# Performance work log

Measured on AMD Instinct MI355X. Metric: run time of the kernel, lower is better.

## Reference

```python
import jax, jax.numpy as jnp
import numpy as np

HID = 256

def lstm_cell(x, h, c, Wih, Whh, bih, bhh):
    # PyTorch LSTM gate order: i, f, g, o
    g = x @ Wih.T + h @ Whh.T + bih + bhh
    i, f, gg, o = jnp.split(g, 4, axis=-1)
    c = jax.nn.sigmoid(f) * c + jax.nn.sigmoid(i) * jnp.tanh(gg)
    h = jax.nn.sigmoid(o) * jnp.tanh(c)
    return h, c

def lstm_seq(x, Wih, Whh, bih, bhh):
    # x: [B, T, D] -> outputs [B, T, H], final (h, c)
    B = x.shape[0]
    h0 = jnp.zeros((B, HID), x.dtype)
    def step(carry, xt):
        h, c = lstm_cell(xt, carry[0], carry[1], Wih, Whh, bih, bhh)
        return (h, c), h
    (h, c), ys = jax.lax.scan(step, (h0, h0), jnp.swapaxes(x, 0, 1))
    return jnp.swapaxes(ys, 0, 1), h, c

def setup_inputs():
    key = jax.random.key(0)
    B, M, H_WIN, NTH, NTW = 512, 16, 25, 64, 64
    SAL = NTH * NTW
    ks = iter(jax.random.split(key, 40))
    def U(shape):
        return jax.random.uniform(next(ks), shape, jnp.float32, -0.0625, 0.0625)
    def lstm_p(pfx, din):
        return {pfx + '_Wih': U((4 * HID, din)), pfx + '_Whh': U((4 * HID, HID)),
                pfx + '_bih': U((4 * HID,)), pfx + '_bhh': U((4 * HID,))}
    inp = {
        'encoder_position_inputs': jax.random.normal(next(ks), (B, M, 3), jnp.float32) * 0.1,
        'encoder_saliency_inputs': jax.random.uniform(next(ks), (B, M, NTH, NTW), jnp.float32),
        'decoder_position_inputs': jax.random.normal(next(ks), (B, 1, 3), jnp.float32) * 0.1,
        'decoder_saliency_inputs': jax.random.uniform(next(ks), (B, H_WIN, NTH, NTW), jnp.float32),
    }
    for pfx, din in [('pe', 3), ('se', SAL), ('fe', 2 * HID), ('pd', 3), ('sd', SAL), ('fd', 2 * HID)]:
        inp.update(lstm_p(pfx, din))
    inp['f2_W'] = U((HID, HID)); inp['f2_b'] = U((HID,))
    inp['out_W'] = U((3, HID)); inp['out_b'] = U((3,))
    return inp

def reference(encoder_position_inputs, encoder_saliency_inputs, decoder_position_inputs, decoder_saliency_inputs,
              pe_Wih, pe_Whh, pe_bih, pe_bhh, se_Wih, se_Whh, se_bih, se_bhh,
              fe_Wih, fe_Whh, fe_bih, fe_bhh, pd_Wih, pd_Whh, pd_bih, pd_bhh,
              sd_Wih, sd_Whh, sd_bih, sd_bhh, fd_Wih, fd_Whh, fd_bih, fd_bhh,
              f2_W, f2_b, out_W, out_b):
    B, M = encoder_position_inputs.shape[:2]
    SAL = encoder_saliency_inputs.shape[2] * encoder_saliency_inputs.shape[3]
    # encoder
    out_pos, h1, c1 = lstm_seq(encoder_position_inputs, pe_Wih, pe_Whh, pe_bih, pe_bhh)
    out_sal, h2, c2 = lstm_seq(encoder_saliency_inputs.reshape(B, M, SAL), se_Wih, se_Whh, se_bih, se_bhh)
    conc_enc = jnp.concatenate([out_sal, out_pos], axis=-1)
    _, hf, cf = lstm_seq(conc_enc, fe_Wih, fe_Whh, fe_bih, fe_bhh)
    # decoder: H_WINDOW single-step recurrence; fuse LSTM restarts from (hf, cf) every step
    dec_sal = decoder_saliency_inputs.reshape(B, -1, SAL)
    def step(carry, sal_t):
        inp, h1, c1, h2, c2 = carry
        h1, c1 = lstm_cell(inp, h1, c1, pd_Wih, pd_Whh, pd_bih, pd_bhh)
        h2, c2 = lstm_cell(sal_t, h2, c2, sd_Wih, sd_Whh, sd_bih, sd_bhh)
        conc = jnp.concatenate([h2, h1], axis=-1)
        hfd, _ = lstm_cell(conc, hf, cf, fd_Wih, fd_Whh, fd_bih, fd_bhh)
        fuse2 = hfd @ f2_W.T + f2_b
        delta = fuse2 @ out_W.T + out_b
        pred = inp + delta  # toPosition: orientation + motion
        return (pred, h1, c1, h2, c2), pred
    init = (decoder_position_inputs[:, 0], h1, c1, h2, c2)
    _, preds = jax.lax.scan(step, init, jnp.swapaxes(dec_sal, 0, 1))
    return jnp.swapaxes(preds, 0, 1)  # [B, H_WINDOW, 3]
```

## Files before the change

### kernel.cpp

```cpp
#include <hip/hip_runtime.h>

#define HID 256
#define BATCH 512
#define MENC 16
#define HWIN 25
#define SALSZ 4096
#define BH (BATCH * HID)

typedef __attribute__((ext_vector_type(8))) short bf16x8;
typedef __attribute__((ext_vector_type(4))) float f32x4;

__device__ __forceinline__ float sigmf(float x) { return 1.0f / (1.0f + __expf(-x)); }
__device__ __forceinline__ ushort f2bf(float f) {
    uint32_t u = __float_as_uint(f);
    return (ushort)((u + 0x7fffu + ((u >> 16) & 1u)) >> 16);
}

#define GLOAD_LDS(gp, lp) \
    __builtin_amdgcn_global_load_lds((const __attribute__((address_space(1))) void*)(gp), \
                                     (__attribute__((address_space(3))) void*)(lp), 16, 0, 0)

__device__ __forceinline__ void st_u64(void* p, unsigned long long v) {
    __hip_atomic_store((unsigned long long*)p, v, __ATOMIC_RELAXED, __HIP_MEMORY_SCOPE_AGENT);
}
__device__ __forceinline__ void st_f32(float* p, float v) {
    __hip_atomic_store(p, v, __ATOMIC_RELAXED, __HIP_MEMORY_SCOPE_AGENT);
}

__device__ __forceinline__ void gbar_arrive(unsigned int* slot)
{
    __syncthreads();
    if (threadIdx.x == 0) atomicAdd(slot, 1u);
}
__device__ __forceinline__ void gbar_wait(unsigned int* slot, unsigned int nblk)
{
    if (threadIdx.x == 0) {
        while (__hip_atomic_load(slot, __ATOMIC_RELAXED, __HIP_MEMORY_SCOPE_AGENT) < nblk)
            __builtin_amdgcn_s_sleep(1);
    }
    __syncthreads();
}

__device__ __forceinline__ void stage_wtile(const ushort* Wsrc, int ldw, int u0,
                                            ushort* lds, int lane, int wq)
{
    const int sub = lane >> 5, uu = lane & 31;
#pragma unroll
    for (int i = 0; i < 8; ++i) {
        const int row = i * 8 + wq * 2 + sub;
        const int su  = uu ^ (row & 7);
        const int gr  = (row >> 4) * HID + u0 + (row & 15);
        GLOAD_LDS(Wsrc + (size_t)gr * ldw + su * 8, lds + i * 2048 + wq * 512);
    }
}

__device__ __forceinline__ void cell_g(const ushort* hrow0, int ldh,
                                       const ushort* WsL, f32x4 acc[4], int lane)
{
    const int fr = lane & 15, fq = lane >> 4;
    const ushort* hrow = hrow0 + (size_t)fr * ldh;
#pragma unroll
    for (int ks = 0; ks < 8; ++ks) {
        const bf16x8 af = *(const bf16x8*)(hrow + ks * 32 + fq * 8);
#pragma unroll
        for (int g = 0; g < 4; ++g) {
            const int vr = g * 16 + fr;
            const bf16x8 bf = *(const bf16x8*)(WsL + vr * 256 + (((ks * 4 + fq)) ^ (vr & 7)) * 8);
            acc[g] = __builtin_amdgcn_mfma_f32_16x16x32_bf16(af, bf, acc[g], 0, 0, 0);
        }
    }
}

struct Cvt9 {
    const float* s[9];
    ushort*      d[9];
    int          end[9];
};
__global__ __launch_bounds__(256)
void cvt_multi(Cvt9 A)
{
    int i = blockIdx.x * 256 + threadIdx.x;
    if (i >= A.end[8]) return;
    int seg = 0, beg = 0;
#pragma unroll
    for (int k = 0; k < 8; ++k)
        if (i >= A.end[k]) { seg = k + 1; beg = A.end[k]; }
    const int j = i - beg;
    const float4 v = *(const float4*)(A.s[seg] + (size_t)j * 4);
    *(ushort4*)(A.d[seg] + (size_t)j * 4) = make_ushort4(f2bf(v.x), f2bf(v.y), f2bf(v.z), f2bf(v.w));
}

__device__ __forceinline__ void loadA128(const float* Ag, int lda, int tid, float4 ra[4])
{
#pragma unroll
    for (int j = 0; j < 2; ++j) {
        const int idx = j * 512 + tid;
        const int row = idx >> 3, u = idx & 7;
        const int su = (u ^ (row & 7)) * 8;
        ra[2 * j + 0] = *(const float4*)(Ag + (size_t)row * lda + su);
        ra[2 * j + 1] = *(const float4*)(Ag + (size_t)row * lda + su + 4);
    }
}
__device__ __forceinline__ void writeA128(const float4 ra[4], ushort* Al, int tid)
{
#pragma unroll
    for (int j = 0; j < 2; ++j) {
        const int idx = j * 512 + tid;
        uint4 v;
        v.x = (uint)f2bf(ra[2 * j].x) | ((uint)f2bf(ra[2 * j].y) << 16);
        v.y = (uint)f2bf(ra[2 * j].z) | ((uint)f2bf(ra[2 * j].w) << 16);
        v.z = (uint)f2bf(ra[2 * j + 1].x) | ((uint)f2bf(ra[2 * j + 1].y) << 16);
        v.w = (uint)f2bf(ra[2 * j + 1].z) | ((uint)f2bf(ra[2 * j + 1].w) << 16);
        *(uint4*)(Al + idx * 8) = v;
    }
}
__device__ __forceinline__ void stageB128(const ushort* Bg, int ldw, ushort* Bl, int tid)
{
#pragma unroll
    for (int j = 0; j < 2; ++j) {
        const int idx = j * 512 + tid;
        const int row = idx >> 3, u = idx & 7;
        const int su = (u ^ (row & 7)) * 8;
        GLOAD_LDS(Bg + (size_t)row * ldw + su, Bl + idx * 8);
    }
}

__device__ __forceinline__ void gemm128f_body(
    const float* __restrict__ A, const ushort* __restrict__ W, float* __restrict__ C,
    int lda, int ldw, int ldc, int K, int gx, int nwg, int bid,
    ushort* AsB, ushort* BsB, int tid)
{
    const int lane = tid & 63, wid = tid >> 6;
    {
        const int q = nwg >> 3, r = nwg & 7;
        const int xcd = bid & 7, o = bid >> 3;
        bid = (xcd < r) ? xcd * (q + 1) + o : r * (q + 1) + (xcd - r) * q + o;
    }
    const int m0 = (bid / gx) * 128, n0 = (bid % gx) * 128;

    const int wr = wid >> 1, wc = wid & 1;
    const int fr = lane & 15, fq = lane >> 4;

    f32x4 acc[2][4] = {};
    const int nt = K / 64;
    const float*  Ab0 = A + (size_t)m0 * lda;
    const ushort* Bb0 = W + (size_t)n0 * ldw;

    float4 ra[4];
    loadA128(Ab0, lda, tid, ra);
    stageB128(Bb0, ldw, BsB, tid);
    writeA128(ra, AsB, tid);
    loadA128(Ab0 + 64, lda, tid, ra);
    asm volatile("s_waitcnt vmcnt(4) lgkmcnt(0)" ::: "memory");
    __builtin_amdgcn_sched_barrier(0);
    __builtin_amdgcn_s_barrier();
    __builtin_amdgcn_sched_barrier(0);

    for (int t = 0; t < nt; ++t) {
        const int p = t & 1;
        const int t1 = (t + 1 < nt) ? t + 1 : nt - 1;
        const int t2 = (t + 2 < nt) ? t + 2 : nt - 1;
        stageB128(Bb0 + t1 * 64, ldw, BsB + (p ^ 1) * 8192, tid);
        writeA128(ra, AsB + (p ^ 1) * 8192, tid);
        loadA128(Ab0 + t2 * 64, lda, tid, ra);

        const ushort* Ab = AsB + p * 8192;
        const ushort* Bb = BsB + p * 8192;
#pragma unroll
        for (int ks = 0; ks < 2; ++ks) {
            bf16x8 bfr[4];
#pragma unroll
            for (int nf = 0; nf < 4; ++nf) {
                const int row = wc * 64 + nf * 16 + fr;
                bfr[nf] = *(const bf16x8*)(Bb + row * 64 + ((ks * 4 + fq) ^ (row & 7)) * 8);
            }
            bf16x8 af[2];
#pragma unroll
            for (int mf = 0; mf < 2; ++mf) {
                const int row = wr * 32 + mf * 16 + fr;
                af[mf] = *(const bf16x8*)(Ab + row * 64 + ((ks * 4 + fq) ^ (row & 7)) * 8);
            }
            __builtin_amdgcn_s_setprio(1);
#pragma unroll
            for (int mf = 0; mf < 2; ++mf)
#pragma unroll
                for (int nf = 0; nf < 4; ++nf)
                    acc[mf][nf] = __builtin_amdgcn_mfma_f32_16x16x32_bf16(
                        af[mf], bfr[nf], acc[mf][nf], 0, 0, 0);
            __builtin_amdgcn_s_setprio(0);
        }
        if (t == nt - 1) break;
        asm volatile("s_waitcnt vmcnt(4) lgkmcnt(0)" ::: "memory");
        __builtin_amdgcn_sched_barrier(0);
        __builtin_amdgcn_s_barrier();
        __builtin_amdgcn_sched_barrier(0);
    }

    const int cl = lane & 15, ch = lane >> 4;
#pragma unroll
    for (int mf = 0; mf < 2; ++mf)
#pragma unroll
        for (int nf = 0; nf < 4; ++nf)
#pragma unroll
            for (int r = 0; r < 4; ++r)
                C[(size_t)(m0 + wr * 32 + mf * 16 + ch * 4 + r) * ldc
                  + n0 + wc * 64 + nf * 16 + cl] = acc[mf][nf][r];
}

__global__ __launch_bounds__(512, 4)
void gemm128f(const float* __restrict__ A, const ushort* __restrict__ W,
              float* __restrict__ C, int gx, int nwg)
{
    __shared__ ushort As[2 * 128 * 64];
    __shared__ ushort Bs[2 * 128 * 64];
    gemm128f_body(A, W, C, SALSZ, SALSZ, 1024, SALSZ, gx, nwg, blockIdx.x, As, Bs, threadIdx.x);
}

__device__ __forceinline__ void gemm128b_body(
    const ushort* __restrict__ A, const ushort* __restrict__ W, float* __restrict__ C,
    int lda, int ldw, int ldc, int K, int gx, int nwg, int bid,
    const float* __restrict__ rbias, unsigned int* flag,
    ushort* AsB, ushort* BsB, int tid)
{
    const int lane = tid & 63, wid = tid >> 6;
    {
        const int q = nwg >> 3, r = nwg & 7;
        const int xcd = bid & 7, o = bid >> 3;
        bid = (xcd < r) ? xcd * (q + 1) + o : r * (q + 1) + (xcd - r) * q + o;
    }
    const int m0 = (bid / gx) * 128, n0 = (bid % gx) * 128;

    const int wr = wid >> 1, wc = wid & 1;
    const int fr = lane & 15, fq = lane >> 4;

    f32x4 acc[2][4] = {};
    const int nt = K / 64;
    const ushort* Ab0 = A + (size_t)m0 * lda;
    const ushort* Bb0 = W + (size_t)n0 * ldw;

    stageB128(Ab0, lda, AsB, tid);
    stageB128(Bb0, ldw, BsB, tid);
    __syncthreads();

    for (int t = 0; t < nt; ++t) {
        const int p = t & 1;
        if (t + 1 < nt) {
            stageB128(Ab0 + (t + 1) * 64, lda, AsB + (p ^ 1) * 8192, tid);
            stageB128(Bb0 + (t + 1) * 64, ldw, BsB + (p ^ 1) * 8192, tid);
        }
        const ushort* Ab = AsB + p * 8192;
        const ushort* Bb = BsB + p * 8192;
#pragma unroll
        for (int ks = 0; ks < 2; ++ks) {
            bf16x8 bfr[4];
#pragma unroll
            for (int nf = 0; nf < 4; ++nf) {
                const int row = wc * 64 + nf * 16 + fr;
                bfr[nf] = *(const bf16x8*)(Bb + row * 64 + ((ks * 4 + fq) ^ (row & 7)) * 8);
            }
            bf16x8 af[2];
#pragma unroll
            for (int mf = 0; mf < 2; ++mf) {
                const int row = wr * 32 + mf * 16 + fr;
                af[mf] = *(const bf16x8*)(Ab + row * 64 + ((ks * 4 + fq) ^ (row & 7)) * 8);
            }
#pragma unroll
            for (int mf = 0; mf < 2; ++mf)
#pragma unroll
                for (int nf = 0; nf < 4; ++nf)
                    acc[mf][nf] = __builtin_amdgcn_mfma_f32_16x16x32_bf16(
                        af[mf], bfr[nf], acc[mf][nf], 0, 0, 0);
        }
        if (t == nt - 1) break;
        __syncthreads();
    }

    const int cl = lane & 15, ch = lane >> 4;
#pragma unroll
    for (int mf = 0; mf < 2; ++mf)
#pragma unroll
        for (int nf = 0; nf < 4; ++nf)
#pragma unroll
            for (int r = 0; r < 4; ++r) {
                const int mm = m0 + wr * 32 + mf * 16 + ch * 4 + r;
                const int nn = n0 + wc * 64 + nf * 16 + cl;
                float v = acc[mf][nf][r];
                if (rbias) v += rbias[(size_t)(mm & 511) * ldc + nn];
                st_f32(C + (size_t)mm * ldc + nn, v);
            }
    __syncthreads();
    if (tid == 0) atomicAdd(flag + (m0 >> 9), 1u);
}

struct EncArgs {
    const ushort *WHse, *WHpe;
    const float  *xg_se;
    const float  *enc_pos;
    const float  *se_b1, *se_b2, *pe_b1, *pe_b2;
    const float  *pe_Wih;
    ushort       *conc;
    float        *SE_C, *PE_C;
    unsigned int *bar;
};

__global__ __launch_bounds__(512, 4)
void enc_sd(EncArgs A, const float* __restrict__ sdA, const ushort* __restrict__ sdW,
            float* __restrict__ sdC)
{
    __shared__ ushort sh[34816];
    const int tid = threadIdx.x;

    if (blockIdx.x >= 128) {
        gemm128f_body(sdA, sdW, sdC, SALSZ, SALSZ, 1024, SALSZ, 8, 800,
                      (int)blockIdx.x - 128, sh, sh + 16384, tid);
        return;
    }

    const int lane = tid & 63, w = tid >> 6;
    const int role  = blockIdx.x >> 6;
    const int rem   = blockIdx.x & 63;
    const int btile = rem & 7, usup = rem >> 3;
    const int b0 = btile * 64, ub = usup * 32;
    const int usub = w & 1, bsub = w >> 1;
    const int u0t = ub + usub * 16;
    const int grp = role * 8 + btile;
    const int fr = lane & 15, fq = lane >> 4;
    const int u = u0t + fr;
    const int ul = usub * 16 + fr;
    const int coff = role ? 256 : 0;
    ushort* Ws0 = sh + usub * 16384;
    ushort (*hloc)[32] = (ushort(*)[32])(sh + 32768);

    stage_wtile(role ? A.WHpe : A.WHse, HID, u0t, Ws0, lane, bsub);

    const float* b1 = role ? A.pe_b1 : A.se_b1;
    const float* b2 = role ? A.pe_b2 : A.se_b2;
    float bias[4], wxs[4][3];
#pragma unroll
    for (int g = 0; g < 4; ++g) {
        bias[g] = b1[g * HID + u] + b2[g * HID + u];
        wxs[g][0] = wxs[g][1] = wxs[g][2] = 0.0f;
        if (role) {
            wxs[g][0] = A.pe_Wih[(g * HID + u) * 3 + 0];
            wxs[g][1] = A.pe_Wih[(g * HID + u) * 3 + 1];
            wxs[g][2] = A.pe_Wih[(g * HID + u) * 3 + 2];
        }
    }
    float c[4] = {0.f, 0.f, 0.f, 0.f};
    __syncthreads();

    for (int t = 0; t < MENC; ++t) {
        float xg[4][4];
#pragma unroll
        for (int r = 0; r < 4; ++r) {
            const int b = b0 + bsub * 16 + fq * 4 + r;
            if (role) {
                const float* xp = A.enc_pos + ((size_t)b * MENC + t) * 3;
                xg[r][0] = xp[0]; xg[r][1] = xp[1]; xg[r][2] = xp[2]; xg[r][3] = 0.f;
            } else {
#pragma unroll
                for (int g = 0; g < 4; ++g)
                    xg[r][g] = A.xg_se[((size_t)b * MENC + t) * 1024 + g * HID + u];
            }
        }
        if (t > 0) gbar_wait(A.bar + grp * MENC + (t - 1), 8);
        f32x4 acc[4] = {};
        if (t > 0)
            cell_g(A.conc + ((size_t)(t - 1) * 512 + b0 + bsub * 16) * 512 + coff, 512,
                   Ws0, acc, lane);
#pragma unroll
        for (int r = 0; r < 4; ++r) {
            const int bl = bsub * 16 + fq * 4 + r;
            const int b = b0 + bl;
            float gv[4];
#pragma unroll
            for (int g = 0; g < 4; ++g) {
                float v = acc[g][r] + bias[g];
                if (role) v += xg[r][0] * wxs[g][0] + xg[r][1] * wxs[g][1] + xg[r][2] * wxs[g][2];
                else      v += xg[r][g];
                gv[g] = v;
            }
            const float cn = sigmf(gv[1]) * c[r] + sigmf(gv[0]) * tanhf(gv[2]);
            const float hn = sigmf(gv[3]) * tanhf(cn);
            c[r] = cn;
            hloc[bl][ul] = f2bf(hn);
            if (t == MENC - 1) (role ? A.PE_C : A.SE_C)[(size_t)b * HID + u] = cn;
        }
        __syncthreads();
        {
            const int row = tid >> 3, c8 = tid & 7;
            const unsigned long long v = *(const unsigned long long*)&hloc[row][c8 * 4];
            st_u64(A.conc + ((size_t)t * 512 + b0 + row) * 512 + coff + ub + c8 * 4, v);
        }
        if (t != MENC - 1) gbar_arrive(A.bar + grp * MENC + t);
    }
}

struct MidArgs {
    const ushort *WHsd, *WHfe;
    const float  *xg_sd;
    const float  *xg_fe;
    const float  *sd_b1, *sd_b2, *fe_b1, *fe_b2;
    const ushort *conc;
    const float  *SE_C;
    ushort       *SDB;
    ushort       *FEB;
    float        *FEH, *FE_C;
    unsigned int *bar;
    unsigned int *fe_done;
};

__global__ __launch_bounds__(512, 4)
void mid_fe(MidArgs A, const ushort* __restrict__ feA, const ushort* __restrict__ feW,
            float* __restrict__ feC)
{
    __shared__ ushort sh[34816];
    const int tid = threadIdx.x;

    if (blockIdx.x >= 128) {
        gemm128b_body(feA, feW, feC, 512, 512, 1024, 512, 8, 512,
                      (int)blockIdx.x - 128, nullptr, A.fe_done, sh, sh + 16384, tid);
        return;
    }

    const int lane = tid & 63, w = tid >> 6;
    const int role  = blockIdx.x >> 6;
    const int rem   = blockIdx.x & 63;
    const int btile = rem & 7, usup = rem >> 3;
    const int b0 = btile * 64, ub = usup * 32;
    const int usub = w & 1, bsub = w >> 1;
    const int u0t = ub + usub * 16;
    const int grp = role * 8 + btile;
    const int fr = lane & 15, fq = lane >> 4;
    const int u = u0t + fr;
    const int ul = usub * 16 + fr;
    const int NT = role ? MENC : HWIN;
    ushort* Ws0 = sh + usub * 16384;
    ushort (*hloc)[32] = (ushort(*)[32])(sh + 32768);

    stage_wtile(role ? A.WHfe : A.WHsd, HID, u0t, Ws0, lane, bsub);

    const float* b1 = role ? A.fe_b1 : A.sd_b1;
    const float* b2 = role ? A.fe_b2 : A.sd_b2;
    float bias[4];
#pragma unroll
    for (int g = 0; g < 4; ++g) bias[g] = b1[g * HID + u] + b2[g * HID + u];

    float c[4];
#pragma unroll
    for (int r = 0; r < 4; ++r) {
        const int b = b0 + bsub * 16 + fq * 4 + r;
        c[r] = role ? 0.0f : A.SE_C[(size_t)b * HID + u];
    }
    __syncthreads();

    for (int t = 0; t < NT; ++t) {
        if (role) gbar_wait(A.fe_done + t, 32);
        float xg[4][4];
#pragma unroll
        for (int r = 0; r < 4; ++r) {
            const int b = b0 + bsub * 16 + fq * 4 + r;
#pragma unroll
            for (int g = 0; g < 4; ++g)
                xg[r][g] = role ? A.xg_fe[((size_t)t * 512 + b) * 1024 + g * HID + u]
                                : A.xg_sd[((size_t)b * HWIN + t) * 1024 + g * HID + u];
        }
        if (t > 0) gbar_wait(A.bar + grp * HWIN + (t - 1), 8);
        f32x4 acc[4] = {};
        if (role == 0) {
            if (t == 0) cell_g(A.conc + ((size_t)15 * 512 + b0 + bsub * 16) * 512, 512,
                               Ws0, acc, lane);
            else        cell_g(A.SDB + ((size_t)(t - 1) * 512 + b0 + bsub * 16) * HID, HID,
                               Ws0, acc, lane);
        } else if (t > 0) {
            cell_g(A.FEB + ((size_t)(t - 1) * BATCH + b0 + bsub * 16) * HID, HID,
                   Ws0, acc, lane);
        }
#pragma unroll
        for (int r = 0; r < 4; ++r) {
            const int bl = bsub * 16 + fq * 4 + r;
            const int b = b0 + bl;
            float gv[4];
#pragma unroll
            for (int g = 0; g < 4; ++g)
                gv[g] = acc[g][r] + bias[g] + xg[r][g];
            const float cn = sigmf(gv[1]) * c[r] + sigmf(gv[0]) * tanhf(gv[2]);
            const float hn = sigmf(gv[3]) * tanhf(cn);
            c[r] = cn;
            hloc[bl][ul] = f2bf(hn);
            if (role == 1 && t == MENC - 1) {
                A.FEH[(size_t)b * HID + u] = hn;
                A.FE_C[(size_t)b * HID + u] = cn;
            }
        }
        __syncthreads();
        {
            const int row = tid >> 3, c8 = tid & 7;
            const unsigned long long v = *(const unsigned long long*)&hloc[row][c8 * 4];
            ushort* dst = role ? (A.FEB + ((size_t)t * BATCH + b0 + row) * 256 + ub + c8 * 4)
                               : (A.SDB + ((size_t)t * 512 + b0 + row) * 256 + ub + c8 * 4);
            st_u64(dst, v);
        }
        if (t != NT - 1) gbar_arrive(A.bar + grp * HWIN + t);
    }
}

__global__ __launch_bounds__(256)
void gemm_tn(const float* __restrict__ A, const float* __restrict__ W,
             const float* __restrict__ b1, const float* __restrict__ b2,
             float* __restrict__ C,
             int M, int N, int K, int lda, int ldw, int ldc)
{
    __shared__ float AsT[16][68];
    __shared__ float WsT[16][68];
    const int t  = threadIdx.x;
    const int tx = t & 15, ty = t >> 4;
    const int m0 = blockIdx.y * 64, n0 = blockIdx.x * 64;
    const int lr = t >> 2;
    const int c4 = t & 3;

    float acc[4][4];
#pragma unroll
    for (int i = 0; i < 4; ++i)
#pragma unroll
        for (int j = 0; j < 4; ++j) acc[i][j] = 0.0f;

    for (int k0 = 0; k0 < K; k0 += 16) {
        float a[4], w[4];
        const int kb = k0 + c4 * 4;
#pragma unroll
        for (int k = 0; k < 4; ++k) {
            a[k] = (kb + k < K) ? A[(size_t)(m0 + lr) * lda + kb + k] : 0.0f;
            w[k] = (kb + k < K) ? W[(size_t)(n0 + lr) * ldw + kb + k] : 0.0f;
        }
        __syncthreads();
#pragma unroll
        for (int k = 0; k < 4; ++k) {
            AsT[c4 * 4 + k][lr] = a[k];
            WsT[c4 * 4 + k][lr] = w[k];
        }
        __syncthreads();
#pragma unroll
        for (int kk = 0; kk < 16; ++kk) {
            const float4 av = *(const float4*)&AsT[kk][ty * 4];
            const float4 wv = *(const float4*)&WsT[kk][tx * 4];
            acc[0][0] += av.x * wv.x; acc[0][1] += av.x * wv.y; acc[0][2] += av.x * wv.z; acc[0][3] += av.x * wv.w;
            acc[1][0] += av.y * wv.x; acc[1][1] += av.y * wv.y; acc[1][2] += av.y * wv.z; acc[1][3] += av.y * wv.w;
            acc[2][0] += av.z * wv.x; acc[2][1] += av.z * wv.y; acc[2][2] += av.z * wv.z; acc[2][3] += av.z * wv.w;
            acc[3][0] += av.w * wv.x; acc[3][1] += av.w * wv.y; acc[3][2] += av.w * wv.z; acc[3][3] += av.w * wv.w;
        }
    }

#pragma unroll
    for (int i = 0; i < 4; ++i) {
        const int m = m0 + ty * 4 + i;
#pragma unroll
        for (int j = 0; j < 4; ++j) {
            const int n = n0 + tx * 4 + j;
            float v = acc[i][j];
            if (b1) v += b1[n];
            if (b2) v += b2[n];
            C[(size_t)m * ldc + n] = v;
        }
    }
}

struct DecArgs {
    const ushort *WHpd;
    const ushort *WFDh;
    const ushort *peF;
    const float  *PE_C, *FE_C;
    const float  *xh2;
    const float  *pd_b1, *pd_b2, *pd_Wih;
    const float  *G, *c3, *dec_pos;
    ushort       *H1;
    float        *DELTA;
    float        *out;
    unsigned int *bar;
    unsigned int *xh2_done;
};

__global__ __launch_bounds__(512)
void dec_xh2(DecArgs A, const ushort* __restrict__ xA, const ushort* __restrict__ xW,
             float* __restrict__ xC, const float* __restrict__ xrb)
{
    __shared__ ushort sh[68096];
    const int tid = threadIdx.x;

    if (blockIdx.x >= 64) {
        gemm128b_body(xA, xW, xC, 256, 512, 1024, 256, 8, 800,
                      (int)blockIdx.x - 64, xrb, A.xh2_done, sh, sh + 16384, tid);
        return;
    }

    ushort* Wpd0 = sh;
    ushort* Wfd0 = sh + 32768;
    ushort (*hloc)[32] = (ushort(*)[32])(sh + 65536);
    float* pred_lds = (float*)(sh + 67584);

    const int lane = tid & 63, w = tid >> 6;
    const int btile = blockIdx.x & 7, usup = blockIdx.x >> 3;
    const int b0 = btile * 64, ub = usup * 32;
    const int usub = w & 1, bsub = w >> 1;
    const int u0t = ub + usub * 16;
    const int fr = lane & 15, fq = lane >> 4;
    const int u = u0t + fr;
    const int ul = usub * 16 + fr;
    unsigned int* bars = A.bar + btile * 2 * HWIN;

    stage_wtile(A.WHpd, HID, u0t, Wpd0 + usub * 16384, lane, bsub);
    stage_wtile(A.WFDh, 512, u0t, Wfd0 + usub * 16384, lane, bsub);

    float pdb[4], wxs[4][3], cf[4], c1[4], Gu[3];
#pragma unroll
    for (int g = 0; g < 4; ++g) {
        pdb[g] = A.pd_b1[g * HID + u] + A.pd_b2[g * HID + u];
        wxs[g][0] = A.pd_Wih[(g * HID + u) * 3 + 0];
        wxs[g][1] = A.pd_Wih[(g * HID + u) * 3 + 1];
        wxs[g][2] = A.pd_Wih[(g * HID + u) * 3 + 2];
    }
#pragma unroll
    for (int r = 0; r < 4; ++r) {
        const int b = b0 + bsub * 16 + fq * 4 + r;
        c1[r] = A.PE_C[(size_t)b * HID + u];
        cf[r] = A.FE_C[(size_t)b * HID + u];
    }
    Gu[0] = A.G[0 * HID + u]; Gu[1] = A.G[1 * HID + u]; Gu[2] = A.G[2 * HID + u];
    const float c3r = (tid < 192) ? A.c3[tid % 3] : 0.0f;
    if (tid < 192) pred_lds[tid] = A.dec_pos[(size_t)(b0 + tid / 3) * 3 + tid % 3];
    __syncthreads();

    for (int t = 0; t < HWIN; ++t) {
        f32x4 acc[4] = {};
        if (t == 0) cell_g(A.peF + (size_t)(b0 + bsub * 16) * 512, 512,
                           Wpd0 + usub * 16384, acc, lane);
        else        cell_g(A.H1 + ((size_t)(t - 1) * BATCH + b0 + bsub * 16) * HID, HID,
                           Wpd0 + usub * 16384, acc, lane);
        if (t > 0) {
            gbar_wait(bars + 2 * (t - 1) + 1, 8);
            if (tid < 192) {
                pred_lds[tid] += A.DELTA[((size_t)(t - 1) * 512 + b0 + tid / 3) * 3 + tid % 3] + c3r;
                if (usup == 0)
                    A.out[((size_t)(b0 + tid / 3) * HWIN + (t - 1)) * 3 + tid % 3] = pred_lds[tid];
            }
            __syncthreads();
        }
#pragma unroll
        for (int r = 0; r < 4; ++r) {
            const int bl = bsub * 16 + fq * 4 + r;
            const float x0 = pred_lds[bl * 3 + 0];
            const float x1 = pred_lds[bl * 3 + 1];
            const float x2 = pred_lds[bl * 3 + 2];
            float gv[4];
#pragma unroll
            for (int g = 0; g < 4; ++g)
                gv[g] = acc[g][r] + pdb[g] + x0 * wxs[g][0] + x1 * wxs[g][1] + x2 * wxs[g][2];
            const float cn = sigmf(gv[1]) * c1[r] + sigmf(gv[0]) * tanhf(gv[2]);
            const float hn = sigmf(gv[3]) * tanhf(cn);
            c1[r] = cn;
            hloc[bl][ul] = f2bf(hn);
        }
        __syncthreads();
        {
            const int row = tid >> 3, c8 = tid & 7;
            const unsigned long long v = *(const unsigned long long*)&hloc[row][c8 * 4];
            st_u64(A.H1 + ((size_t)t * BATCH + b0 + row) * 256 + ub + c8 * 4, v);
        }
        gbar_arrive(bars + 2 * t);
        gbar_wait(A.xh2_done + t, 32);
        float xh[4][4];
#pragma unroll
        for (int r = 0; r < 4; ++r) {
            const int b = b0 + bsub * 16 + fq * 4 + r;
#pragma unroll
            for (int g = 0; g < 4; ++g)
                xh[r][g] = A.xh2[((size_t)t * 512 + b) * 1024 + g * HID + u];
        }
        gbar_wait(bars + 2 * t, 8);
        {
            f32x4 accB[4] = {};
            cell_g(A.H1 + ((size_t)t * BATCH + b0 + bsub * 16) * HID, HID,
                   Wfd0 + usub * 16384, accB, lane);
#pragma unroll
            for (int r = 0; r < 4; ++r) {
                const int b = b0 + bsub * 16 + fq * 4 + r;
                float gv[4];
#pragma unroll
                for (int g = 0; g < 4; ++g)
                    gv[g] = accB[g][r] + xh[r][g];
                const float cn = sigmf(gv[1]) * cf[r] + sigmf(gv[0]) * tanhf(gv[2]);
                const float hn = sigmf(gv[3]) * tanhf(cn);
                float p0 = hn * Gu[0], p1 = hn * Gu[1], p2 = hn * Gu[2];
#pragma unroll
                for (int s = 1; s < 16; s <<= 1) {
                    p0 += __shfl_xor(p0, s);
                    p1 += __shfl_xor(p1, s);
                    p2 += __shfl_xor(p2, s);
                }
                if (fr == 0) {
                    float* d = A.DELTA + ((size_t)t * 512 + b) * 3;
                    atomicAdd(d + 0, p0); atomicAdd(d + 1, p1); atomicAdd(d + 2, p2);
                }
            }
        }
        gbar_arrive(bars + 2 * t + 1);
    }
    gbar_wait(bars + 2 * (HWIN - 1) + 1, 8);
    if (tid < 192) {
        pred_lds[tid] += A.DELTA[((size_t)(HWIN - 1) * 512 + b0 + tid / 3) * 3 + tid % 3] + c3r;
        if (usup == 0)
            A.out[((size_t)(b0 + tid / 3) * HWIN + (HWIN - 1)) * 3 + tid % 3] = pred_lds[tid];
    }
}

__global__ __launch_bounds__(256)
void precompute_G(const float* __restrict__ f2W, const float* __restrict__ f2b,
                  const float* __restrict__ outW, const float* __restrict__ outb,
                  float* __restrict__ G, float* __restrict__ c3)
{
    const int k = threadIdx.x;
    float g0 = 0.f, g1 = 0.f, g2 = 0.f;
    for (int n = 0; n < HID; ++n) {
        const float w = f2W[n * HID + k];
        g0 += outW[n] * w;
        g1 += outW[HID + n] * w;
        g2 += outW[2 * HID + n] * w;
    }
    G[k] = g0; G[HID + k] = g1; G[2 * HID + k] = g2;
    if (k < 3) {
        float s = outb[k];
        for (int n = 0; n < HID; ++n) s += outW[k * HID + n] * f2b[n];
        c3[k] = s;
    }
}

extern "C" void kernel_launch(void* const* d_in, const int* in_sizes, int n_in,
                              void* d_out, int out_size, void* d_ws, size_t ws_size,
                              hipStream_t stream)
{
    (void)in_sizes; (void)n_in; (void)out_size; (void)ws_size;
    const float* enc_pos = (const float*)d_in[0];
    const float* enc_sal = (const float*)d_in[1];
    const float* dec_pos = (const float*)d_in[2];
    const float* dec_sal = (const float*)d_in[3];
    const float *pe_Wih = (const float*)d_in[4],  *pe_Whh = (const float*)d_in[5],
                *pe_bih = (const float*)d_in[6],  *pe_bhh = (const float*)d_in[7];
    const float *se_Wih = (const float*)d_in[8],  *se_Whh = (const float*)d_in[9],
                *se_bih = (const float*)d_in[10], *se_bhh = (const float*)d_in[11];
    const float *fe_Wih = (const float*)d_in[12], *fe_Whh = (const float*)d_in[13],
                *fe_bih = (const float*)d_in[14], *fe_bhh = (const float*)d_in[15];
    const float *pd_Wih = (const float*)d_in[16], *pd_Whh = (const float*)d_in[17],
                *pd_bih = (const float*)d_in[18], *pd_bhh = (const float*)d_in[19];
    const float *sd_Wih = (const float*)d_in[20], *sd_Whh = (const float*)d_in[21],
                *sd_bih = (const float*)d_in[22], *sd_bhh = (const float*)d_in[23];
    const float *fd_Wih = (const float*)d_in[24], *fd_Whh = (const float*)d_in[25],
                *fd_bih = (const float*)d_in[26], *fd_bhh = (const float*)d_in[27];
    const float *f2_W = (const float*)d_in[28], *f2_b = (const float*)d_in[29];
    const float *out_W = (const float*)d_in[30], *out_b = (const float*)d_in[31];
    float* out = (float*)d_out;
    float* ws  = (float*)d_ws;

    size_t off = 0;
    float* XG_SE = ws + off; off += (size_t)8192 * 1024;
    float* XG_FE = ws + off; off += (size_t)8192 * 1024;
    float* BIG   = ws + off; off += (size_t)12800 * 1024;
    float* BIG2  = ws + off; off += (size_t)12800 * 1024;
    float* GBIAS = ws + off; off += (size_t)BATCH * 1024;
    float* PE_C  = ws + off; off += BH;
    float* SE_C  = ws + off; off += BH;
    float* FE_C  = ws + off; off += BH;
    float* FEH   = ws + off; off += BH;
    float* Gm    = ws + off; off += 1024;
    float* C3    = ws + off; off += 8;
    float* DELTA = ws + off; off += (size_t)HWIN * BATCH * 3 + 64;
    unsigned int* BAR = (unsigned int*)(ws + off); off += 1280;
    ushort* WSE  = (ushort*)(ws + off); off += ((size_t)1024 * 4096) / 2;
    ushort* WSD  = (ushort*)(ws + off); off += ((size_t)1024 * 4096) / 2;
    ushort* WFE  = (ushort*)(ws + off); off += ((size_t)1024 * 512) / 2;
    ushort* WFD  = (ushort*)(ws + off); off += ((size_t)1024 * 512) / 2;
    ushort* WHpe = (ushort*)(ws + off); off += ((size_t)1024 * 256) / 2;
    ushort* WHse = (ushort*)(ws + off); off += ((size_t)1024 * 256) / 2;
    ushort* WHfe = (ushort*)(ws + off); off += ((size_t)1024 * 256) / 2;
    ushort* WHsd = (ushort*)(ws + off); off += ((size_t)1024 * 256) / 2;
    ushort* WHpd = (ushort*)(ws + off); off += ((size_t)1024 * 256) / 2;
    ushort* CONC = (ushort*)(ws + off); off += ((size_t)MENC * 512 * 512) / 2;
    ushort* SDB  = (ushort*)(ws + off); off += ((size_t)HWIN * BH) / 2;
    ushort* FEB  = (ushort*)(ws + off); off += ((size_t)MENC * BH) / 2;
    ushort* H1   = (ushort*)(ws + off); off += ((size_t)HWIN * BH) / 2;

    unsigned int* FE_DONE  = BAR + 1100;
    unsigned int* XH2_DONE = BAR + 1128;

    hipMemsetAsync(DELTA, 0, ((size_t)HWIN * BATCH * 3 + 64 + 1280) * 4, stream);

    {
        Cvt9 a;
        const float* srcs[9] = { se_Wih, sd_Wih, fe_Wih, fd_Wih, pe_Whh, se_Whh, fe_Whh, sd_Whh, pd_Whh };
        ushort*      dsts[9] = { WSE,    WSD,    WFE,    WFD,    WHpe,   WHse,   WHfe,   WHsd,   WHpd };
        const int    n4s[9]  = { 1024*4096/4, 1024*4096/4, 1024*512/4, 1024*512/4,
                                 1024*256/4, 1024*256/4, 1024*256/4, 1024*256/4, 1024*256/4 };
        int acc9 = 0;
        for (int i = 0; i < 9; ++i) { a.s[i] = srcs[i]; a.d[i] = dsts[i]; acc9 += n4s[i]; a.end[i] = acc9; }
        cvt_multi<<<(acc9 + 255) / 256, 256, 0, stream>>>(a);
    }
    precompute_G<<<1, 256, 0, stream>>>(f2_W, f2_b, out_W, out_b, Gm, C3);

    gemm128f<<<512, 512, 0, stream>>>(enc_sal, WSE, XG_SE, 8, 512);

    {
        EncArgs a;
        a.WHse = WHse; a.WHpe = WHpe; a.xg_se = XG_SE; a.enc_pos = enc_pos;
        a.se_b1 = se_bih; a.se_b2 = se_bhh; a.pe_b1 = pe_bih; a.pe_b2 = pe_bhh;
        a.pe_Wih = pe_Wih; a.conc = CONC; a.SE_C = SE_C; a.PE_C = PE_C;
        a.bar = BAR;
        enc_sd<<<928, 512, 0, stream>>>(a, dec_sal, WSD, BIG);
    }

    {
        MidArgs a;
        a.WHsd = WHsd; a.WHfe = WHfe; a.xg_sd = BIG; a.xg_fe = XG_FE;
        a.sd_b1 = sd_bih; a.sd_b2 = sd_bhh; a.fe_b1 = fe_bih; a.fe_b2 = fe_bhh;
        a.conc = CONC; a.SE_C = SE_C; a.SDB = SDB; a.FEB = FEB;
        a.FEH = FEH; a.FE_C = FE_C; a.bar = BAR + 256; a.fe_done = FE_DONE;
        mid_fe<<<640, 512, 0, stream>>>(a, CONC, WFE, XG_FE);
    }

    gemm_tn<<<dim3(16, 8), 256, 0, stream>>>(FEH, fd_Whh, fd_bih, fd_bhh, GBIAS,
                                             BATCH, 1024, HID, HID, HID, 1024);

    {
        DecArgs a;
        a.WHpd = WHpd; a.WFDh = WFD + 256;
        a.peF = CONC + ((size_t)15 * 512) * 512 + 256;
        a.PE_C = PE_C; a.FE_C = FE_C; a.xh2 = BIG2;
        a.pd_b1 = pd_bih; a.pd_b2 = pd_bhh; a.pd_Wih = pd_Wih;
        a.G = Gm; a.c3 = C3; a.dec_pos = dec_pos;
        a.H1 = H1; a.DELTA = DELTA; a.out = out; a.bar = BAR + 656;
        a.xh2_done = XH2_DONE;
        dec_xh2<<<864, 512, 0, stream>>>(a, SDB, WFD, BIG2, GBIAS);
    }
}
```

Measured before the change: 964.1 us.

## Move decoder xh2 GEMM into mid kernel, gated on per-step SDB flags

The decoder's x@W GEMM over the saliency-decoder hidden states now runs inside the mid kernel as extra workgroups. Each workgroup waits on a per-timestep counter that the SD recurrence bumps, so the GEMM overlaps the recurrence instead of the decoder chain. The decoder becomes a lean 64-block kernel that holds the fuse-decoder bias (GBIAS) in registers and adds it itself, no longer waiting on the xh2 flags. The cost is a larger mid-kernel grid, spin-waiting GEMM blocks that may hold CU slots while the recurrence runs, and an extra syncthreads plus atomic per recurrence step.

```diff
diff --git a/kernel.cpp b/kernel.cpp
--- a/kernel.cpp
+++ b/kernel.cpp
@@ -219,7 +219,7 @@
 __device__ __forceinline__ void gemm128b_body(
     const ushort* __restrict__ A, const ushort* __restrict__ W, float* __restrict__ C,
     int lda, int ldw, int ldc, int K, int gx, int nwg, int bid,
-    const float* __restrict__ rbias, unsigned int* flag,
+    unsigned int* wflag, unsigned int wcnt, unsigned int* sflag, bool wt,
     ushort* AsB, ushort* BsB, int tid)
 {
     const int lane = tid & 63, wid = tid >> 6;
@@ -230,6 +230,8 @@
     }
     const int m0 = (bid / gx) * 128, n0 = (bid % gx) * 128;
 
+    if (wflag) gbar_wait(wflag + (m0 >> 9), wcnt);
+
     const int wr = wid >> 1, wc = wid & 1;
     const int fr = lane & 15, fq = lane >> 4;
 
@@ -284,12 +286,13 @@
             for (int r = 0; r < 4; ++r) {
                 const int mm = m0 + wr * 32 + mf * 16 + ch * 4 + r;
                 const int nn = n0 + wc * 64 + nf * 16 + cl;
-                float v = acc[mf][nf][r];
-                if (rbias) v += rbias[(size_t)(mm & 511) * ldc + nn];
-                st_f32(C + (size_t)mm * ldc + nn, v);
-            }
-    __syncthreads();
-    if (tid == 0) atomicAdd(flag + (m0 >> 9), 1u);
+                if (wt) st_f32(C + (size_t)mm * ldc + nn, acc[mf][nf][r]);
+                else    C[(size_t)mm * ldc + nn] = acc[mf][nf][r];
+            }
+    if (sflag) {
+        __syncthreads();
+        if (tid == 0) atomicAdd(sflag + (m0 >> 9), 1u);
+    }
 }
 
 struct EncArgs {
@@ -408,18 +411,28 @@
     float        *FEH, *FE_C;
     unsigned int *bar;
     unsigned int *fe_done;
+    unsigned int *sdb_done;
 };
 
 __global__ __launch_bounds__(512, 4)
-void mid_fe(MidArgs A, const ushort* __restrict__ feA, const ushort* __restrict__ feW,
-            float* __restrict__ feC)
+void mid_fe_xh2(MidArgs A, const ushort* __restrict__ feA, const ushort* __restrict__ feW,
+                float* __restrict__ feC,
+                const ushort* __restrict__ xA, const ushort* __restrict__ xW,
+                float* __restrict__ xC)
 {
     __shared__ ushort sh[34816];
     const int tid = threadIdx.x;
 
+    if (blockIdx.x >= 640) {
+        gemm128b_body(xA, xW, xC, 256, 512, 1024, 256, 8, 800,
+                      (int)blockIdx.x - 640, A.sdb_done, 64, nullptr, false,
+                      sh, sh + 16384, tid);
+        return;
+    }
     if (blockIdx.x >= 128) {
         gemm128b_body(feA, feW, feC, 512, 512, 1024, 512, 8, 512,
-                      (int)blockIdx.x - 128, nullptr, A.fe_done, sh, sh + 16384, tid);
+                      (int)blockIdx.x - 128, nullptr, 0, A.fe_done, true,
+                      sh, sh + 16384, tid);
         return;
     }
 
@@ -501,7 +514,11 @@
                                : (A.SDB + ((size_t)t * 512 + b0 + row) * 256 + ub + c8 * 4);
             st_u64(dst, v);
         }
-        if (t != NT - 1) gbar_arrive(A.bar + grp * HWIN + t);
+        __syncthreads();
+        if (tid == 0) {
+            if (role == 0) atomicAdd(A.sdb_done + t, 1u);
+            if (t != NT - 1) atomicAdd(A.bar + grp * HWIN + t, 1u);
+        }
     }
 }
 
@@ -569,7 +586,7 @@
     const ushort *WHpd;
     const ushort *WFDh;
     const ushort *peF;
-    const float  *PE_C, *FE_C;
+    const float  *PE_C, *FE_C, *GBIAS;
     const float  *xh2;
     const float  *pd_b1, *pd_b2, *pd_Wih;
     const float  *G, *c3, *dec_pos;
@@ -577,28 +594,15 @@
     float        *DELTA;
     float        *out;
     unsigned int *bar;
-    unsigned int *xh2_done;
 };
 
 __global__ __launch_bounds__(512)
-void dec_xh2(DecArgs A, const ushort* __restrict__ xA, const ushort* __restrict__ xW,
-             float* __restrict__ xC, const float* __restrict__ xrb)
-{
-    __shared__ ushort sh[68096];
-    const int tid = threadIdx.x;
-
-    if (blockIdx.x >= 64) {
-        gemm128b_body(xA, xW, xC, 256, 512, 1024, 256, 8, 800,
-                      (int)blockIdx.x - 64, xrb, A.xh2_done, sh, sh + 16384, tid);
-        return;
-    }
-
-    ushort* Wpd0 = sh;
-    ushort* Wfd0 = sh + 32768;
-    ushort (*hloc)[32] = (ushort(*)[32])(sh + 65536);
-    float* pred_lds = (float*)(sh + 67584);
-
-    const int lane = tid & 63, w = tid >> 6;
+void dec_chain(DecArgs A)
+{
+    __shared__ ushort Wpd[2][64 * 256], Wfd[2][64 * 256];
+    __shared__ ushort hloc[64][32];
+    __shared__ float pred_lds[192];
+    const int tid = threadIdx.x, lane = tid & 63, w = tid >> 6;
     const int btile = blockIdx.x & 7, usup = blockIdx.x >> 3;
     const int b0 = btile * 64, ub = usup * 32;
     const int usub = w & 1, bsub = w >> 1;
@@ -608,10 +612,10 @@
     const int ul = usub * 16 + fr;
     unsigned int* bars = A.bar + btile * 2 * HWIN;
 
-    stage_wtile(A.WHpd, HID, u0t, Wpd0 + usub * 16384, lane, bsub);
-    stage_wtile(A.WFDh, 512, u0t, Wfd0 + usub * 16384, lane, bsub);
-
-    float pdb[4], wxs[4][3], cf[4], c1[4], Gu[3];
+    stage_wtile(A.WHpd, HID, u0t, Wpd[usub], lane, bsub);
+    stage_wtile(A.WFDh, 512, u0t, Wfd[usub], lane, bsub);
+
+    float pdb[4], wxs[4][3], cf[4], c1[4], Gu[3], gb[4][4];
 #pragma unroll
     for (int g = 0; g < 4; ++g) {
         pdb[g] = A.pd_b1[g * HID + u] + A.pd_b2[g * HID + u];
@@ -624,6 +628,8 @@
         const int b = b0 + bsub * 16 + fq * 4 + r;
         c1[r] = A.PE_C[(size_t)b * HID + u];
         cf[r] = A.FE_C[(size_t)b * HID + u];
+#pragma unroll
+        for (int g = 0; g < 4; ++g) gb[r][g] = A.GBIAS[(size_t)b * 1024 + g * HID + u];
     }
     Gu[0] = A.G[0 * HID + u]; Gu[1] = A.G[1 * HID + u]; Gu[2] = A.G[2 * HID + u];
     const float c3r = (tid < 192) ? A.c3[tid % 3] : 0.0f;
@@ -632,10 +638,9 @@
 
     for (int t = 0; t < HWIN; ++t) {
         f32x4 acc[4] = {};
-        if (t == 0) cell_g(A.peF + (size_t)(b0 + bsub * 16) * 512, 512,
-                           Wpd0 + usub * 16384, acc, lane);
+        if (t == 0) cell_g(A.peF + (size_t)(b0 + bsub * 16) * 512, 512, Wpd[usub], acc, lane);
         else        cell_g(A.H1 + ((size_t)(t - 1) * BATCH + b0 + bsub * 16) * HID, HID,
-                           Wpd0 + usub * 16384, acc, lane);
+                           Wpd[usub], acc, lane);
         if (t > 0) {
             gbar_wait(bars + 2 * (t - 1) + 1, 8);
             if (tid < 192) {
@@ -667,7 +672,6 @@
             st_u64(A.H1 + ((size_t)t * BATCH + b0 + row) * 256 + ub + c8 * 4, v);
         }
         gbar_arrive(bars + 2 * t);
-        gbar_wait(A.xh2_done + t, 32);
         float xh[4][4];
 #pragma unroll
         for (int r = 0; r < 4; ++r) {
@@ -680,14 +684,14 @@
         {
             f32x4 accB[4] = {};
             cell_g(A.H1 + ((size_t)t * BATCH + b0 + bsub * 16) * HID, HID,
-                   Wfd0 + usub * 16384, accB, lane);
+                   Wfd[usub], accB, lane);
 #pragma unroll
             for (int r = 0; r < 4; ++r) {
                 const int b = b0 + bsub * 16 + fq * 4 + r;
                 float gv[4];
 #pragma unroll
                 for (int g = 0; g < 4; ++g)
-                    gv[g] = accB[g][r] + xh[r][g];
+                    gv[g] = accB[g][r] + xh[r][g] + gb[r][g];
                 const float cn = sigmf(gv[1]) * cf[r] + sigmf(gv[0]) * tanhf(gv[2]);
                 const float hn = sigmf(gv[3]) * tanhf(cn);
                 float p0 = hn * Gu[0], p1 = hn * Gu[1], p2 = hn * Gu[2];
@@ -789,7 +793,7 @@
     ushort* H1   = (ushort*)(ws + off); off += ((size_t)HWIN * BH) / 2;
 
     unsigned int* FE_DONE  = BAR + 1100;
-    unsigned int* XH2_DONE = BAR + 1128;
+    unsigned int* SDB_DONE = BAR + 1160;
 
     hipMemsetAsync(DELTA, 0, ((size_t)HWIN * BATCH * 3 + 64 + 1280) * 4, stream);
 
@@ -821,8 +825,9 @@
         a.WHsd = WHsd; a.WHfe = WHfe; a.xg_sd = BIG; a.xg_fe = XG_FE;
         a.sd_b1 = sd_bih; a.sd_b2 = sd_bhh; a.fe_b1 = fe_bih; a.fe_b2 = fe_bhh;
         a.conc = CONC; a.SE_C = SE_C; a.SDB = SDB; a.FEB = FEB;
-        a.FEH = FEH; a.FE_C = FE_C; a.bar = BAR + 256; a.fe_done = FE_DONE;
-        mid_fe<<<640, 512, 0, stream>>>(a, CONC, WFE, XG_FE);
+        a.FEH = FEH; a.FE_C = FE_C; a.bar = BAR + 256;
+        a.fe_done = FE_DONE; a.sdb_done = SDB_DONE;
+        mid_fe_xh2<<<1440, 512, 0, stream>>>(a, CONC, WFE, XG_FE, SDB, WFD, BIG2);
     }
 
     gemm_tn<<<dim3(16, 8), 256, 0, stream>>>(FEH, fd_Whh, fd_bih, fd_bhh, GBIAS,
@@ -832,11 +837,10 @@
         DecArgs a;
         a.WHpd = WHpd; a.WFDh = WFD + 256;
         a.peF = CONC + ((size_t)15 * 512) * 512 + 256;
-        a.PE_C = PE_C; a.FE_C = FE_C; a.xh2 = BIG2;
+        a.PE_C = PE_C; a.FE_C = FE_C; a.GBIAS = GBIAS; a.xh2 = BIG2;
         a.pd_b1 = pd_bih; a.pd_b2 = pd_bhh; a.pd_Wih = pd_Wih;
         a.G = Gm; a.c3 = C3; a.dec_pos = dec_pos;
         a.H1 = H1; a.DELTA = DELTA; a.out = out; a.bar = BAR + 656;
-        a.xh2_done = XH2_DONE;
-        dec_xh2<<<864, 512, 0, stream>>>(a, SDB, WFD, BIG2, GBIAS);
-    }
-}
+        dec_chain<<<64, 512, 0, stream>>>(a);
+    }
+}
```

After: 957.1 us. Within noise of the previous version (-0.7%).
